# Kernel optimization log

Measured on AMD Instinct MI355X. Metric: run time of the kernel, lower is better.

The kernel has to match this reference:

```python
import jax, jax.numpy as jnp
import numpy as np

B, H, E = 64, 768, 128


def setup_inputs() -> dict:
    key = jax.random.key(0)
    k0, k1, k2, k3, k4, k5 = jax.random.split(key, 6)
    s = 1.0 / np.sqrt(H).astype(np.float32)
    return {
        "head_src": jax.random.normal(k0, (B, H), dtype=jnp.float32),
        "rel_src": jax.random.normal(k1, (B, H), dtype=jnp.float32),
        "tail_src": jax.random.normal(k2, (B, H), dtype=jnp.float32),
        "W_e": jax.random.normal(k3, (E, H), dtype=jnp.float32) * s,
        "b_e": jnp.zeros((E,), dtype=jnp.float32),
        "W_r": jax.random.normal(k4, (E, H), dtype=jnp.float32) * s,
        "b_r": jnp.zeros((E,), dtype=jnp.float32),
        # core tensor init mirrors np.random.uniform(-1, 1, (E, E, E))
        "core": jax.random.uniform(k5, (E, E, E), dtype=jnp.float32, minval=-1.0, maxval=1.0),
    }


def reference(head_src, rel_src, tail_src, W_e, b_e, W_r, b_r, core):
    # forward(): entity / relation projections (nn.Linear)
    head = head_src @ W_e.T + b_e          # [B, E]
    tail = tail_src @ W_e.T + b_e          # [B, E]
    rel = rel_src @ W_r.T + b_r            # [B, E]

    # energy(): faithful replication of the broadcast multiply+sum sequence.
    # head/rel/tail all broadcast along core dim 0 due to the unsqueeze pattern.
    w = (core[None] * head[:, :, None, None]).sum(-1)   # [B, E, E] (via [B,E,E,E] intermediate)
    w = (w * rel[:, :, None]).sum(-1)                   # [B, E]
    energy = -(w * tail).sum(-1)                        # [B]
    return energy
```

## Files before the change

kernel.cpp:

```cpp
#include <hip/hip_runtime.h>

#define HDIM 768
#define EDIM 128
#define BDIM 64

#define NCORE_BLOCKS 1024
#define NPROJ_BLOCKS 768

__global__ __launch_bounds__(256) void fused_kernel(
    const float* __restrict__ core,
    const float* __restrict__ head_src, const float* __restrict__ rel_src,
    const float* __restrict__ tail_src,
    const float* __restrict__ W_e, const float* __restrict__ b_e,
    const float* __restrict__ W_r, const float* __restrict__ b_r,
    float* __restrict__ partials, float* __restrict__ P) {
    __shared__ float wpart[4];
    const int blk = blockIdx.x;
    const int t = threadIdx.x;
    const int wave = t >> 6, lane = t & 63;

    if (blk < NCORE_BLOCKS) {
        const int i     = blk >> 3;
        const int chunk = blk & 7;
        const float4* p = (const float4*)(core + (size_t)i * 16384 + (size_t)chunk * 2048);
        float4 a = p[t];
        float4 b = p[t + 256];
        float s = (a.x + a.y) + (a.z + a.w) + (b.x + b.y) + (b.z + b.w);
        for (int off = 32; off; off >>= 1) s += __shfl_down(s, off, 64);
        if (lane == 0) wpart[wave] = s;
        __syncthreads();
        if (t == 0) partials[blk] = (wpart[0] + wpart[1]) + (wpart[2] + wpart[3]);
    } else {
        const int pid = blk - NCORE_BLOCKS;
        const int wg  = pid * 4 + wave;
        const int ich = wg & 15;
        const int mb  = wg >> 4;
        const int m   = mb >> 6;
        const int b   = mb & 63;

        const float* src  = (m == 0) ? head_src : (m == 1) ? rel_src : tail_src;
        const float* W    = (m == 1) ? W_r : W_e;
        const float* bias = (m == 1) ? b_r : b_e;

        const float4* s4 = (const float4*)(src + b * HDIM);
        const float4 x0 = s4[lane], x1 = s4[lane + 64], x2 = s4[lane + 128];

        const int i0 = ich * 8;
#pragma unroll
        for (int u = 0; u < 8; ++u) {
            const int i = i0 + u;
            const float4* w4 = (const float4*)(W + i * HDIM);
            const float4 w0 = w4[lane], w1 = w4[lane + 64], w2 = w4[lane + 128];
            float d = w0.x * x0.x + w0.y * x0.y + w0.z * x0.z + w0.w * x0.w
                    + w1.x * x1.x + w1.y * x1.y + w1.z * x1.z + w1.w * x1.w
                    + w2.x * x2.x + w2.y * x2.y + w2.z * x2.z + w2.w * x2.w;
            for (int off = 32; off; off >>= 1) d += __shfl_down(d, off, 64);
            if (lane == 0) P[(m * BDIM + b) * EDIM + i] = d + bias[i];
        }
    }
}

__global__ __launch_bounds__(128) void final_kernel(
    const float* __restrict__ partials, const float* __restrict__ P,
    float* __restrict__ out) {
    const int b = blockIdx.x;
    const int i = threadIdx.x;

    float S = 0.f;
#pragma unroll
    for (int c = 0; c < 8; ++c) S += partials[i * 8 + c];

    const float h = P[(0 * BDIM + b) * EDIM + i];
    const float r = P[(1 * BDIM + b) * EDIM + i];
    const float tt = P[(2 * BDIM + b) * EDIM + i];
    float val = S * h * r * tt;

    for (int off = 32; off; off >>= 1) val += __shfl_down(val, off, 64);
    __shared__ float wsum[2];
    if ((i & 63) == 0) wsum[i >> 6] = val;
    __syncthreads();
    if (i == 0) out[b] = -(wsum[0] + wsum[1]);
}

extern "C" void kernel_launch(void* const* d_in, const int* in_sizes, int n_in,
                              void* d_out, int out_size, void* d_ws, size_t ws_size,
                              hipStream_t stream) {
    const float* head_src = (const float*)d_in[0];
    const float* rel_src  = (const float*)d_in[1];
    const float* tail_src = (const float*)d_in[2];
    const float* W_e      = (const float*)d_in[3];
    const float* b_e      = (const float*)d_in[4];
    const float* W_r      = (const float*)d_in[5];
    const float* b_r      = (const float*)d_in[6];
    const float* core     = (const float*)d_in[7];
    float* out      = (float*)d_out;
    float* partials = (float*)d_ws;
    float* P        = (float*)d_ws + NCORE_BLOCKS;

    fused_kernel<<<NCORE_BLOCKS + NPROJ_BLOCKS, 256, 0, stream>>>(
        core, head_src, rel_src, tail_src, W_e, b_e, W_r, b_r, partials, P);
    final_kernel<<<BDIM, 128, 0, stream>>>(partials, P, out);
}
```

Measured before the change: 79.48 us.

## Fuse final reduction into main kernel via last-block atomic counter

Replaces the second launch with a last-block-done pattern: each block increments an atomic counter after its writes, and the final block computes the per-batch energies from the projections and core partial sums. The core reduction also uses fewer, larger blocks (256 instead of 1024), each loading eight float4 per thread. This is meant to remove a kernel launch and the gap between launches. In exchange it adds a memset launch, threadfences, and serial tail work done by a single block.

```diff
diff --git a/kernel.cpp b/kernel.cpp
--- a/kernel.cpp
+++ b/kernel.cpp
@@ -4,37 +4,48 @@
 #define EDIM 128
 #define BDIM 64
 
-#define NCORE_BLOCKS 1024
+#define NCORE_BLOCKS 256
 #define NPROJ_BLOCKS 768
+#define NGRID (NCORE_BLOCKS + NPROJ_BLOCKS)
 
-__global__ __launch_bounds__(256) void fused_kernel(
+#define WS_PARTIALS 64
+#define WS_P 1024
+
+__global__ __launch_bounds__(256) void tucker_kernel(
     const float* __restrict__ core,
     const float* __restrict__ head_src, const float* __restrict__ rel_src,
     const float* __restrict__ tail_src,
     const float* __restrict__ W_e, const float* __restrict__ b_e,
     const float* __restrict__ W_r, const float* __restrict__ b_r,
-    float* __restrict__ partials, float* __restrict__ P) {
-    __shared__ float wpart[4];
+    float* __restrict__ ws, float* __restrict__ out) {
+    float* partials = ws + WS_PARTIALS;
+    float* P        = ws + WS_P;
+    unsigned* cnt   = (unsigned*)ws;
+
     const int blk = blockIdx.x;
     const int t = threadIdx.x;
     const int wave = t >> 6, lane = t & 63;
 
+    __shared__ float wpart[4];
+    __shared__ int is_last;
+
     if (blk < NCORE_BLOCKS) {
-        const int i     = blk >> 3;
-        const int chunk = blk & 7;
-        const float4* p = (const float4*)(core + (size_t)i * 16384 + (size_t)chunk * 2048);
-        float4 a = p[t];
-        float4 b = p[t + 256];
-        float s = (a.x + a.y) + (a.z + a.w) + (b.x + b.y) + (b.z + b.w);
+        const int i = blk >> 1, h = blk & 1;
+        const float4* p = (const float4*)(core + (size_t)i * 16384 + (size_t)h * 8192);
+        float4 v0 = p[t], v1 = p[t + 256], v2 = p[t + 512], v3 = p[t + 768];
+        float4 v4 = p[t + 1024], v5 = p[t + 1280], v6 = p[t + 1536], v7 = p[t + 1792];
+        float s = ((v0.x + v0.y) + (v0.z + v0.w)) + ((v1.x + v1.y) + (v1.z + v1.w))
+                + ((v2.x + v2.y) + (v2.z + v2.w)) + ((v3.x + v3.y) + (v3.z + v3.w))
+                + ((v4.x + v4.y) + (v4.z + v4.w)) + ((v5.x + v5.y) + (v5.z + v5.w))
+                + ((v6.x + v6.y) + (v6.z + v6.w)) + ((v7.x + v7.y) + (v7.z + v7.w));
         for (int off = 32; off; off >>= 1) s += __shfl_down(s, off, 64);
         if (lane == 0) wpart[wave] = s;
         __syncthreads();
         if (t == 0) partials[blk] = (wpart[0] + wpart[1]) + (wpart[2] + wpart[3]);
     } else {
-        const int pid = blk - NCORE_BLOCKS;
-        const int wg  = pid * 4 + wave;
-        const int ich = wg & 15;
-        const int mb  = wg >> 4;
+        const int wt  = (blk - NCORE_BLOCKS) * 4 + wave;
+        const int ich = wt & 15;
+        const int mb  = wt >> 4;
         const int m   = mb >> 6;
         const int b   = mb & 63;
 
@@ -57,29 +68,32 @@
             for (int off = 32; off; off >>= 1) d += __shfl_down(d, off, 64);
             if (lane == 0) P[(m * BDIM + b) * EDIM + i] = d + bias[i];
         }
+        __syncthreads();
     }
-}
 
-__global__ __launch_bounds__(128) void final_kernel(
-    const float* __restrict__ partials, const float* __restrict__ P,
-    float* __restrict__ out) {
-    const int b = blockIdx.x;
-    const int i = threadIdx.x;
+    if (t == 0) {
+        __threadfence();
+        unsigned old = atomicAdd(cnt, 1u);
+        is_last = (old == NGRID - 1);
+    }
+    __syncthreads();
+    if (!is_last) return;
+    __threadfence();
 
-    float S = 0.f;
-#pragma unroll
-    for (int c = 0; c < 8; ++c) S += partials[i * 8 + c];
+    __shared__ float s_S[EDIM];
+    if (t < EDIM) s_S[t] = partials[2 * t] + partials[2 * t + 1];
+    __syncthreads();
 
-    const float h = P[(0 * BDIM + b) * EDIM + i];
-    const float r = P[(1 * BDIM + b) * EDIM + i];
-    const float tt = P[(2 * BDIM + b) * EDIM + i];
-    float val = S * h * r * tt;
-
-    for (int off = 32; off; off >>= 1) val += __shfl_down(val, off, 64);
-    __shared__ float wsum[2];
-    if ((i & 63) == 0) wsum[i >> 6] = val;
-    __syncthreads();
-    if (i == 0) out[b] = -(wsum[0] + wsum[1]);
+    const float* P0 = P;
+    const float* P1 = P + BDIM * EDIM;
+    const float* P2 = P + 2 * BDIM * EDIM;
+    for (int b = wave; b < BDIM; b += 4) {
+        const int i1 = lane, i2 = lane + 64;
+        float v = s_S[i1] * P0[b * EDIM + i1] * P1[b * EDIM + i1] * P2[b * EDIM + i1]
+                + s_S[i2] * P0[b * EDIM + i2] * P1[b * EDIM + i2] * P2[b * EDIM + i2];
+        for (int off = 32; off; off >>= 1) v += __shfl_down(v, off, 64);
+        if (lane == 0) out[b] = -v;
+    }
 }
 
 extern "C" void kernel_launch(void* const* d_in, const int* in_sizes, int n_in,
@@ -93,11 +107,9 @@
     const float* W_r      = (const float*)d_in[5];
     const float* b_r      = (const float*)d_in[6];
     const float* core     = (const float*)d_in[7];
-    float* out      = (float*)d_out;
-    float* partials = (float*)d_ws;
-    float* P        = (float*)d_ws + NCORE_BLOCKS;
 
-    fused_kernel<<<NCORE_BLOCKS + NPROJ_BLOCKS, 256, 0, stream>>>(
-        core, head_src, rel_src, tail_src, W_e, b_e, W_r, b_r, partials, P);
-    final_kernel<<<BDIM, 128, 0, stream>>>(partials, P, out);
+    hipMemsetAsync(d_ws, 0, 4, stream);
+    tucker_kernel<<<NGRID, 256, 0, stream>>>(
+        core, head_src, rel_src, tail_src, W_e, b_e, W_r, b_r,
+        (float*)d_ws, (float*)d_out);
 }
```

Result: slower. 108.0 us (+35.9%).
